# Kernel optimization log

Hardware: AMD Instinct MI355X
Metric: run time of the kernel (lower is better)

Reference implementation:

```python
import jax, jax.numpy as jnp
import numpy as np


def _cdist(p1, p2):
    # Euclidean cdist via the matmul expansion (matches torch.cdist p=2 fast path):
    # ||a-b||^2 = ||a||^2 + ||b||^2 - 2 a.b ; clamp tiny negatives before sqrt.
    sq1 = jnp.sum(p1 * p1, axis=-1, keepdims=True)        # (N, 1)
    sq2 = jnp.sum(p2 * p2, axis=-1, keepdims=True).T      # (1, M)
    d2 = sq1 + sq2 - 2.0 * (p1 @ p2.T)                    # (N, M)
    return jnp.sqrt(jnp.maximum(d2, 0.0))


def setup_inputs() -> dict:
    key = jax.random.key(0)
    k1, k2 = jax.random.split(key)
    N, M = 16384, 16384
    points1 = jax.random.normal(k1, (N, 3), dtype=jnp.float32)
    points2 = jax.random.normal(k2, (M, 3), dtype=jnp.float32)
    return {"points1": points1, "points2": points2}


def reference(points1, points2):
    dist = _cdist(points1, points2)                        # (N, M)
    min1 = jnp.min(dist, axis=1)                           # (N,) nearest in points2
    min2 = jnp.min(dist, axis=0)                           # (M,) nearest in points1
    return jnp.sum(min1) + jnp.sum(min2)
```

## Files before the change

### kernel.cpp

```cpp
#include <hip/hip_runtime.h>
#include <hip/hip_bf16.h>
#include <math.h>


typedef _Float16 half8    __attribute__((ext_vector_type(8)));
typedef float    floatx16 __attribute__((ext_vector_type(16)));

constexpr int CH   = 4096;
constexpr int ROWS = 128;
constexpr int BLK  = 256;

__global__ __launch_bounds__(256) void pack_kernel(
    const float* __restrict__ P1, const float* __restrict__ P2,
    uint2* __restrict__ F1, uint2* __restrict__ F2,
    int n1, int n2, int NP, float* __restrict__ out)
{
    int i = blockIdx.x * 256 + threadIdx.x;
    if (i == 0) out[0] = 0.0f;
    const float* P; uint2* F; int n, idx;
    if (i < NP)          { P = P1; F = F1; n = n1; idx = i; }
    else if (i < 2 * NP) { P = P2; F = F2; n = n2; idx = i - NP; }
    else return;
    int j = idx < n ? idx : n - 1;
    float x = P[3*j], y = P[3*j+1], z = P[3*j+2];
    _Float16 hx = (_Float16)x, hy = (_Float16)y, hz = (_Float16)z;
    float qx = (float)hx, qy = (float)hy, qz = (float)hz;
    _Float16 hw = (_Float16)(qx*qx + qy*qy + qz*qz);
    union { _Float16 h[4]; uint2 u; } p;
    p.h[0] = hx; p.h[1] = hy; p.h[2] = hz; p.h[3] = hw;
    F[idx] = p.u;
}

__global__ __launch_bounds__(BLK, 4) void chamfer_sweep_kernel(
    const uint2* __restrict__ F1, const uint2* __restrict__ F2,
    float* __restrict__ part, int n1, int n2, int YC)
{
    __shared__ uint2 sB[CH];
    __shared__ float sRowMin[ROWS];

    const int dir   = blockIdx.z;
    const uint2* FA = dir == 0 ? F1 : F2;
    const uint2* FB = dir == 0 ? F2 : F1;
    const int nA    = dir == 0 ? n1 : n2;
    float* pbase    = part + (dir == 0 ? 0 : (size_t)YC * n1);

    const int tid  = threadIdx.x;
    const int wave = tid >> 6;
    const int lane = tid & 63;
    const int n    = lane & 31;
    const int g    = lane >> 5;
    const bool g0  = (g == 0);

    {
        const uint4* src = (const uint4*)(FB + (size_t)blockIdx.y * CH);
        uint4* dst = (uint4*)sB;
        for (int i = tid; i < CH / 2; i += BLK) dst[i] = src[i];
    }

    const _Float16 h0 = (_Float16)0.0f;
    half8 af;
    {
        int arow = blockIdx.x * ROWS + wave * 32 + n;
        union { uint2 u; _Float16 h[4]; } au; au.u = FA[arow];
        const _Float16 m2 = (_Float16)(-2.0f);
        af[0] = g0 ? (_Float16)(au.h[0] * m2) : h0;
        af[1] = g0 ? (_Float16)(au.h[1] * m2) : h0;
        af[2] = g0 ? (_Float16)(au.h[2] * m2) : h0;
        af[3] = g0 ? (_Float16)1.0f : h0;
        af[4] = g0 ? au.h[3] : h0;
        af[5] = h0; af[6] = h0; af[7] = h0;
    }

    __syncthreads();

    floatx16 rowmin;
#pragma unroll
    for (int r = 0; r < 16; ++r) rowmin[r] = 1e30f;
    const floatx16 zacc = {};

    union BF { half8 v; unsigned u[4]; uint2 lo; };
    BF bu0, bu1, bu2, bu3;
    { union { _Float16 h[2]; unsigned u; } q;
      q.h[0] = (_Float16)1.0f; q.h[1] = h0;
      bu0.u[2] = q.u; bu0.u[3] = 0u;
      bu1.u[2] = q.u; bu1.u[3] = 0u;
      bu2.u[2] = q.u; bu2.u[3] = 0u;
      bu3.u[2] = q.u; bu3.u[3] = 0u; }

    for (int bt = 0; bt < CH / 128; ++bt) {
        const uint2* p = sB + bt * 128 + n;
        bu0.lo = p[0];
        bu1.lo = p[32];
        bu2.lo = p[64];
        bu3.lo = p[96];

        floatx16 d0 = __builtin_amdgcn_mfma_f32_32x32x16_f16(af, bu0.v, zacc, 0, 0, 0);
        floatx16 d1 = __builtin_amdgcn_mfma_f32_32x32x16_f16(af, bu1.v, zacc, 0, 0, 0);
        floatx16 d2 = __builtin_amdgcn_mfma_f32_32x32x16_f16(af, bu2.v, zacc, 0, 0, 0);
        floatx16 d3 = __builtin_amdgcn_mfma_f32_32x32x16_f16(af, bu3.v, zacc, 0, 0, 0);

#pragma unroll
        for (int r = 0; r < 16; ++r) {
            float t = fminf(fminf(rowmin[r], d0[r]), d1[r]);
            rowmin[r] = fminf(fminf(t, d2[r]), d3[r]);
        }
    }

#pragma unroll
    for (int mask = 1; mask <= 16; mask <<= 1)
#pragma unroll
        for (int r = 0; r < 16; ++r)
            rowmin[r] = fminf(rowmin[r], __shfl_xor(rowmin[r], mask));

    if (n == 0) {
#pragma unroll
        for (int r = 0; r < 16; ++r) {
            int rr = wave * 32 + g * 4 + ((r & 3) + 8 * (r >> 2));
            sRowMin[rr] = rowmin[r];
        }
    }
    __syncthreads();

    if (tid < ROWS) {
        int grow = blockIdx.x * ROWS + tid;
        if (grow < nA) pbase[(size_t)grow * YC + blockIdx.y] = sRowMin[tid];
    }
}

__global__ __launch_bounds__(256) void reduce_kernel(
    const float* __restrict__ part, float* __restrict__ out,
    int ntot, int YC)
{
    __shared__ float s[256];
    int r = blockIdx.x * 256 + threadIdx.x;
    float acc = 0.0f;
    if (r < ntot) {
        float m;
        if (YC == 4) {
            const float4 v = ((const float4*)part)[r];
            m = fminf(fminf(v.x, v.y), fminf(v.z, v.w));
        } else {
            const float* p = part + (size_t)r * YC;
            m = 1e30f;
            for (int y = 0; y < YC; ++y) m = fminf(m, p[y]);
        }
        acc = sqrtf(fmaxf(m, 0.0f));
    }
    s[threadIdx.x] = acc;
    __syncthreads();
    for (int w = 128; w > 0; w >>= 1) {
        if (threadIdx.x < w) s[threadIdx.x] += s[threadIdx.x + w];
        __syncthreads();
    }
    if (threadIdx.x == 0) atomicAdd(out, s[0]);
}

extern "C" void kernel_launch(void* const* d_in, const int* in_sizes, int n_in,
                              void* d_out, int out_size, void* d_ws, size_t ws_size,
                              hipStream_t stream) {
    const float* P1 = (const float*)d_in[0];
    const float* P2 = (const float*)d_in[1];
    const int n1 = in_sizes[0] / 3;
    const int n2 = in_sizes[1] / 3;
    const int nmax = (n1 > n2) ? n1 : n2;
    const int YC = (nmax + CH - 1) / CH;
    const int NP = YC * CH;

    uint2* F1   = (uint2*)d_ws;
    uint2* F2   = F1 + NP;
    float* part = (float*)(F2 + NP);
    float* out  = (float*)d_out;

    pack_kernel<<<(2 * NP + 255) / 256, 256, 0, stream>>>(P1, P2, F1, F2, n1, n2, NP, out);

    {
        dim3 grid(NP / ROWS, YC, 2);
        chamfer_sweep_kernel<<<grid, BLK, 0, stream>>>(F1, F2, part, n1, n2, YC);
    }
    reduce_kernel<<<(n1 + n2 + 255) / 256, 256, 0, stream>>>(part, out, n1 + n2, YC);
}
```

Measured before the change: 77.40 us.

## Switch chamfer sweep to 16x16x32 MFMA with smaller tiles and higher occupancy

After: 85.96 us. +11.1%, slower.

```diff
diff --git a/kernel.cpp b/kernel.cpp
--- a/kernel.cpp
+++ b/kernel.cpp
@@ -4,10 +4,11 @@
 
 
 typedef _Float16 half8    __attribute__((ext_vector_type(8)));
-typedef float    floatx16 __attribute__((ext_vector_type(16)));
+typedef float    floatx4  __attribute__((ext_vector_type(4)));
 
-constexpr int CH   = 4096;
-constexpr int ROWS = 128;
+constexpr int CH   = 2048;
+constexpr int WR   = 16;
+constexpr int ROWS = 64;
 constexpr int BLK  = 256;
 
 __global__ __launch_bounds__(256) void pack_kernel(
@@ -31,7 +32,7 @@
     F[idx] = p.u;
 }
 
-__global__ __launch_bounds__(BLK, 4) void chamfer_sweep_kernel(
+__global__ __launch_bounds__(BLK, 8) void chamfer_sweep_kernel(
     const uint2* __restrict__ F1, const uint2* __restrict__ F2,
     float* __restrict__ part, int n1, int n2, int YC)
 {
@@ -47,9 +48,8 @@
     const int tid  = threadIdx.x;
     const int wave = tid >> 6;
     const int lane = tid & 63;
-    const int n    = lane & 31;
-    const int g    = lane >> 5;
-    const bool g0  = (g == 0);
+    const int n    = lane & 15;
+    const int quad = lane >> 4;
 
     {
         const uint4* src = (const uint4*)(FB + (size_t)blockIdx.y * CH);
@@ -58,25 +58,24 @@
     }
 
     const _Float16 h0 = (_Float16)0.0f;
+    const bool q0 = (quad == 0);
     half8 af;
     {
-        int arow = blockIdx.x * ROWS + wave * 32 + n;
+        int arow = blockIdx.x * ROWS + wave * WR + n;
         union { uint2 u; _Float16 h[4]; } au; au.u = FA[arow];
         const _Float16 m2 = (_Float16)(-2.0f);
-        af[0] = g0 ? (_Float16)(au.h[0] * m2) : h0;
-        af[1] = g0 ? (_Float16)(au.h[1] * m2) : h0;
-        af[2] = g0 ? (_Float16)(au.h[2] * m2) : h0;
-        af[3] = g0 ? (_Float16)1.0f : h0;
-        af[4] = g0 ? au.h[3] : h0;
+        af[0] = q0 ? (_Float16)(au.h[0] * m2) : h0;
+        af[1] = q0 ? (_Float16)(au.h[1] * m2) : h0;
+        af[2] = q0 ? (_Float16)(au.h[2] * m2) : h0;
+        af[3] = q0 ? (_Float16)1.0f : h0;
+        af[4] = q0 ? au.h[3] : h0;
         af[5] = h0; af[6] = h0; af[7] = h0;
     }
 
     __syncthreads();
 
-    floatx16 rowmin;
-#pragma unroll
-    for (int r = 0; r < 16; ++r) rowmin[r] = 1e30f;
-    const floatx16 zacc = {};
+    float rm0 = 1e30f, rm1 = 1e30f, rm2 = 1e30f, rm3 = 1e30f;
+    const floatx4 zacc = {};
 
     union BF { half8 v; unsigned u[4]; uint2 lo; };
     BF bu0, bu1, bu2, bu3;
@@ -87,37 +86,40 @@
       bu2.u[2] = q.u; bu2.u[3] = 0u;
       bu3.u[2] = q.u; bu3.u[3] = 0u; }
 
-    for (int bt = 0; bt < CH / 128; ++bt) {
-        const uint2* p = sB + bt * 128 + n;
+    for (int bt = 0; bt < CH / 64; ++bt) {
+        const uint2* p = sB + bt * 64 + n;
         bu0.lo = p[0];
-        bu1.lo = p[32];
-        bu2.lo = p[64];
-        bu3.lo = p[96];
+        bu1.lo = p[16];
+        bu2.lo = p[32];
+        bu3.lo = p[48];
 
-        floatx16 d0 = __builtin_amdgcn_mfma_f32_32x32x16_f16(af, bu0.v, zacc, 0, 0, 0);
-        floatx16 d1 = __builtin_amdgcn_mfma_f32_32x32x16_f16(af, bu1.v, zacc, 0, 0, 0);
-        floatx16 d2 = __builtin_amdgcn_mfma_f32_32x32x16_f16(af, bu2.v, zacc, 0, 0, 0);
-        floatx16 d3 = __builtin_amdgcn_mfma_f32_32x32x16_f16(af, bu3.v, zacc, 0, 0, 0);
+        floatx4 d0 = __builtin_amdgcn_mfma_f32_16x16x32_f16(af, bu0.v, zacc, 0, 0, 0);
+        floatx4 d1 = __builtin_amdgcn_mfma_f32_16x16x32_f16(af, bu1.v, zacc, 0, 0, 0);
+        floatx4 d2 = __builtin_amdgcn_mfma_f32_16x16x32_f16(af, bu2.v, zacc, 0, 0, 0);
+        floatx4 d3 = __builtin_amdgcn_mfma_f32_16x16x32_f16(af, bu3.v, zacc, 0, 0, 0);
 
-#pragma unroll
-        for (int r = 0; r < 16; ++r) {
-            float t = fminf(fminf(rowmin[r], d0[r]), d1[r]);
-            rowmin[r] = fminf(fminf(t, d2[r]), d3[r]);
-        }
+        float t0 = fminf(fminf(rm0, d0[0]), d1[0]);
+        float t1 = fminf(fminf(rm1, d0[1]), d1[1]);
+        float t2 = fminf(fminf(rm2, d0[2]), d1[2]);
+        float t3 = fminf(fminf(rm3, d0[3]), d1[3]);
+        rm0 = fminf(fminf(t0, d2[0]), d3[0]);
+        rm1 = fminf(fminf(t1, d2[1]), d3[1]);
+        rm2 = fminf(fminf(t2, d2[2]), d3[2]);
+        rm3 = fminf(fminf(t3, d2[3]), d3[3]);
     }
 
 #pragma unroll
-    for (int mask = 1; mask <= 16; mask <<= 1)
-#pragma unroll
-        for (int r = 0; r < 16; ++r)
-            rowmin[r] = fminf(rowmin[r], __shfl_xor(rowmin[r], mask));
-
+    for (int mask = 1; mask <= 8; mask <<= 1) {
+        rm0 = fminf(rm0, __shfl_xor(rm0, mask));
+        rm1 = fminf(rm1, __shfl_xor(rm1, mask));
+        rm2 = fminf(rm2, __shfl_xor(rm2, mask));
+        rm3 = fminf(rm3, __shfl_xor(rm3, mask));
+    }
     if (n == 0) {
-#pragma unroll
-        for (int r = 0; r < 16; ++r) {
-            int rr = wave * 32 + g * 4 + ((r & 3) + 8 * (r >> 2));
-            sRowMin[rr] = rowmin[r];
-        }
+        sRowMin[wave * WR + quad * 4 + 0] = rm0;
+        sRowMin[wave * WR + quad * 4 + 1] = rm1;
+        sRowMin[wave * WR + quad * 4 + 2] = rm2;
+        sRowMin[wave * WR + quad * 4 + 3] = rm3;
     }
     __syncthreads();
 
@@ -136,9 +138,11 @@
     float acc = 0.0f;
     if (r < ntot) {
         float m;
-        if (YC == 4) {
-            const float4 v = ((const float4*)part)[r];
-            m = fminf(fminf(v.x, v.y), fminf(v.z, v.w));
+        if (YC == 8) {
+            const float4* pv = (const float4*)(part + (size_t)r * 8);
+            float4 a = pv[0], b = pv[1];
+            m = fminf(fminf(fminf(a.x, a.y), fminf(a.z, a.w)),
+                      fminf(fminf(b.x, b.y), fminf(b.z, b.w)));
         } else {
             const float* p = part + (size_t)r * YC;
             m = 1e30f;
```
